# Optimization experiments

Measured on AMD Instinct MI355X. Metric: run time of the kernel, lower is better.

The kernel has to match this reference:

```python
import jax, jax.numpy as jnp
import numpy as np
import math

D = 1024
H = 16
B = 4
N = 2048


def setup_inputs() -> dict:
    key = jax.random.key(0)
    ks = jax.random.split(key, 10)
    scale_qkv = 0.01
    def kaiming_uniform(k, shape, scale):
        # attenuated_kaiming_uniform_: fan_in = shape[1], gain for leaky_relu a=sqrt(5)
        fan_in = shape[1]
        gain = math.sqrt(2.0 / (1 + 5.0))
        bound = math.sqrt(3.0) * gain * scale / math.sqrt(fan_in)
        return jax.random.uniform(k, shape, jnp.float32, -bound, bound)
    return {
        "x_q": jax.random.normal(ks[0], (B, N, D), jnp.float32),
        "x_kv": jax.random.normal(ks[1], (B, N, D), jnp.float32),
        "Wq": kaiming_uniform(ks[2], (D, D), scale_qkv),
        "bq": jnp.zeros((D,), jnp.float32),
        "Wk": kaiming_uniform(ks[3], (D, D), scale_qkv),
        "bk": jnp.zeros((D,), jnp.float32),
        "Wv": kaiming_uniform(ks[4], (D, D), scale_qkv),
        "bv": jnp.zeros((D,), jnp.float32),
        "Wo": kaiming_uniform(ks[5], (D, D), 1.0),
        "bo": jnp.zeros((D,), jnp.float32),
    }


def reference(x_q, x_kv, Wq, bq, Wk, bk, Wv, bv, Wo, bo):
    bs, n, d = x_q.shape
    hd = d // H  # head dim
    # torch Linear: y = x @ W^T + b
    q = x_q @ Wq.T + bq
    k = x_kv @ Wk.T + bk
    v = x_kv @ Wv.T + bv
    # reshape to [bs, H, n, hd]
    q = q.reshape(bs, n, H, hd).transpose(0, 2, 1, 3)
    k = k.reshape(bs, n, H, hd).transpose(0, 2, 1, 3)
    v = v.reshape(bs, n, H, hd).transpose(0, 2, 1, 3)
    scores = jnp.einsum("bhqd,bhkd->bhqk", q, k) / math.sqrt(hd)
    seq_ids = jnp.arange(n)
    causal = (seq_ids[None, :] <= seq_ids[:, None]).astype(scores.dtype)  # [n, n]
    scores = scores + (1.0 - causal) * -10000.0
    probs = jax.nn.softmax(scores, axis=-1)
    out = jnp.einsum("bhqk,bhkd->bhqd", probs, v)
    out = out.transpose(0, 2, 1, 3).reshape(bs, n, d)
    return out @ Wo.T + bo
```

## Files before the change

### kernel.cpp

```cpp
#include <hip/hip_runtime.h>

typedef unsigned short u16;
typedef unsigned int u32;
typedef __attribute__((ext_vector_type(8))) short short8;
typedef __attribute__((ext_vector_type(4))) float f32x4;

#define ASYNC_CP16(gsrc, ldst) \
  __builtin_amdgcn_global_load_lds((__attribute__((address_space(1))) void*)(gsrc), \
                                   (__attribute__((address_space(3))) void*)(ldst), 16, 0, 0)

static __device__ __forceinline__ u16 f2bf(float f) {
  u32 u = __builtin_bit_cast(u32, f);
  u = u + 0x7fffu + ((u >> 16) & 1u);
  return (u16)(u >> 16);
}
static __device__ __forceinline__ u32 pk2(float a, float b) {
  return (u32)f2bf(a) | ((u32)f2bf(b) << 16);
}
static __device__ __forceinline__ u32 pk2r(float a, float b) {
  u32 ua = __builtin_bit_cast(u32, a) + 0x8000u;
  u32 ub = __builtin_bit_cast(u32, b) + 0x8000u;
  return __builtin_amdgcn_perm(ub, ua, 0x07060302);
}

__global__ __launch_bounds__(256) void convert_all(
    const float* __restrict__ xq, const float* __restrict__ xkv,
    const float* __restrict__ wq, const float* __restrict__ wk,
    const float* __restrict__ wv, const float* __restrict__ wo,
    u16* __restrict__ dst)
{
  long i = ((long)blockIdx.x * 256 + threadIdx.x) * 4;
  const float* s; long o;
  if      (i < 8388608)  { s = xq;  o = i; }
  else if (i < 16777216) { s = xkv; o = i - 8388608; }
  else if (i < 17825792) { s = wq;  o = i - 16777216; }
  else if (i < 18874368) { s = wk;  o = i - 17825792; }
  else if (i < 19922944) { s = wv;  o = i - 18874368; }
  else                   { s = wo;  o = i - 19922944; }
  float4 v = *(const float4*)(s + o);
  uint2 pkv; pkv.x = pk2(v.x, v.y); pkv.y = pk2(v.z, v.w);
  *(uint2*)(dst + i) = pkv;
}

template<int EPI>
__global__ __launch_bounds__(256)
void gemm_k(const u16* __restrict__ Axq, const u16* __restrict__ Axkv,
            const u16* __restrict__ W0, const u16* __restrict__ W1, const u16* __restrict__ W2,
            const float* __restrict__ b0, const float* __restrict__ b1, const float* __restrict__ b2,
            u16* __restrict__ Qo, u16* __restrict__ Ko, u16* __restrict__ Vo,
            float* __restrict__ Fo)
{
  __shared__ u16 lsa[128*32];
  __shared__ u16 lsb[128*32];
  const int tid = threadIdx.x;
  const int w = tid >> 6, lane = tid & 63;
  const int wr = w >> 1, wc = w & 1;
  const int bm = blockIdx.x, bn = blockIdx.y, z = blockIdx.z;
  const int l15 = lane & 15, l4 = lane >> 4;

  const u16* A; const u16* W; const float* bias;
  if (EPI == 0) {
    A    = (z == 0) ? Axq : Axkv;
    W    = (z == 0) ? W0 : (z == 1) ? W1 : W2;
    bias = (z == 0) ? b0 : (z == 1) ? b1 : b2;
  } else {
    A = Axq; W = W0; bias = b0;
  }
  const u16* Ag = A + (long)bm*128*1024;
  const u16* Wg = W + (long)bn*128*1024;

  f32x4 acc[4][4];
#pragma unroll
  for (int i = 0; i < 4; ++i)
#pragma unroll
    for (int j = 0; j < 4; ++j)
      acc[i][j] = (f32x4){0.f,0.f,0.f,0.f};

  for (int k0 = 0; k0 < 1024; k0 += 32) {
    __syncthreads();
#pragma unroll
    for (int c = 0; c < 2; ++c) {
      int tp = c*256 + tid;
      int row = tp >> 2, col = (tp & 3) * 8;
      ASYNC_CP16(Ag + (long)row*1024 + k0 + col, &lsa[tp*8]);
      ASYNC_CP16(Wg + (long)row*1024 + k0 + col, &lsb[tp*8]);
    }
    __syncthreads();
    short8 af[4], bfr[4];
#pragma unroll
    for (int i = 0; i < 4; ++i)
      af[i] = *(const short8*)&lsa[(wr*64 + i*16 + l15)*32 + l4*8];
#pragma unroll
    for (int j = 0; j < 4; ++j)
      bfr[j] = *(const short8*)&lsb[(wc*64 + j*16 + l15)*32 + l4*8];
#pragma unroll
    for (int i = 0; i < 4; ++i)
#pragma unroll
      for (int j = 0; j < 4; ++j)
        acc[i][j] = __builtin_amdgcn_mfma_f32_16x16x32_bf16(af[i], bfr[j], acc[i][j], 0, 0, 0);
  }

#pragma unroll
  for (int j = 0; j < 4; ++j) {
    const int colg = bn*128 + wc*64 + j*16 + l15;
    const float bb = bias[colg];
#pragma unroll
    for (int i = 0; i < 4; ++i) {
      const int rowg = bm*128 + wr*64 + i*16 + l4*4;
      if (EPI == 1) {
#pragma unroll
        for (int r = 0; r < 4; ++r)
          Fo[(long)(rowg + r)*1024 + colg] = acc[i][j][r] + bb;
      } else {
        const int b  = rowg >> 11, n0 = rowg & 2047;
        const int h  = colg >> 6,  c  = colg & 63;
        const int bh = b*16 + h;
        const long hb = (long)bh*131072 + (long)(n0 >> 7)*8192;
        if (z == 0) {
#pragma unroll
          for (int r = 0; r < 4; ++r)
            Qo[((long)bh*2048 + n0 + r)*64 + c] = f2bf((acc[i][j][r] + bb) * 0.18033688f);
        } else if (z == 1) {
          const long base = hb + (long)(c >> 3)*1024 + (n0 & 127)*8 + (c & 7);
#pragma unroll
          for (int r = 0; r < 4; ++r)
            Ko[base + r*8] = f2bf(acc[i][j][r] + bb);
        } else {
          const long base = hb + (long)((n0 & 127) >> 3)*512 + (long)c*8 + (n0 & 7);
          uint2 pkv;
          pkv.x = pk2(acc[i][j][0] + bb, acc[i][j][1] + bb);
          pkv.y = pk2(acc[i][j][2] + bb, acc[i][j][3] + bb);
          *(uint2*)(Vo + base) = pkv;
        }
      }
    }
  }
}

__global__ __launch_bounds__(256)
void attn_k(const u16* __restrict__ Q, const u16* __restrict__ K,
            const u16* __restrict__ V, u16* __restrict__ AO)
{
  __shared__ u16 lk[8192];
  __shared__ u16 lv[8192];
  __shared__ u16 lp[4][1024];
  const int tid = threadIdx.x;
  const int w = tid >> 6, lane = tid & 63;
  const int l15 = lane & 15, l4 = lane >> 4;
  const int qt = (gridDim.x - 1) - blockIdx.x;
  const int bh = blockIdx.y;
  const int q0 = qt*64;
  const int qg = q0 + w*16 + l15;
  const u16* Qh = Q + (long)bh*131072;
  const u16* Kh = K + (long)bh*131072;
  const u16* Vh = V + (long)bh*131072;

  short8 qf[2];
#pragma unroll
  for (int ks = 0; ks < 2; ++ks)
    qf[ks] = *(const short8*)&Qh[(long)qg*64 + ks*32 + l4*8];

  f32x4 o[4];
#pragma unroll
  for (int nt = 0; nt < 4; ++nt) o[nt] = (f32x4){0.f,0.f,0.f,0.f};
  float rsum = 0.f;

  u16* pw = &lp[w][0];
  const int swz_q = (l15 & 7);
  const int ktmax = (q0 + 63) >> 7;
  for (int kt = 0; kt <= ktmax; ++kt) {
    __syncthreads();
#pragma unroll
    for (int c = 0; c < 4; ++c) {
      int tp = c*256 + tid;
      ASYNC_CP16(Kh + (long)kt*8192 + tp*8, &lk[tp*8]);
      ASYNC_CP16(Vh + (long)kt*8192 + tp*8, &lv[tp*8]);
    }
    __syncthreads();

    f32x4 s[8];
#pragma unroll
    for (int nt = 0; nt < 8; ++nt) s[nt] = (f32x4){0.f,0.f,0.f,0.f};
#pragma unroll
    for (int ks = 0; ks < 2; ++ks)
#pragma unroll
      for (int nt = 0; nt < 8; ++nt) {
        short8 kf = *(const short8*)&lk[(ks*4 + l4)*1024 + (nt*16 + l15)*8];
        s[nt] = __builtin_amdgcn_mfma_f32_16x16x32_bf16(kf, qf[ks], s[nt], 0, 0, 0);
      }

    if (kt*128 + 127 > q0) {
      const int kb = kt*128 + l4*4;
#pragma unroll
      for (int nt = 0; nt < 8; ++nt)
#pragma unroll
        for (int r = 0; r < 4; ++r)
          if (kb + nt*16 + r > qg) s[nt][r] = -1e30f;
    }

    u32 pk[8][2];
#pragma unroll
    for (int nt = 0; nt < 8; ++nt) {
      float p0 = __builtin_amdgcn_exp2f(s[nt][0]);
      float p1 = __builtin_amdgcn_exp2f(s[nt][1]);
      float p2 = __builtin_amdgcn_exp2f(s[nt][2]);
      float p3 = __builtin_amdgcn_exp2f(s[nt][3]);
      rsum += (p0 + p1) + (p2 + p3);
      pk[nt][0] = pk2r(p0, p1);
      pk[nt][1] = pk2r(p2, p3);
    }

#pragma unroll
    for (int h = 0; h < 2; ++h) {
#pragma unroll
      for (int ntl = 0; ntl < 4; ++ntl) {
        const int chunk = ntl*2 + (l4 >> 1);
        const int swz = chunk ^ swz_q;
        uint2 pr; pr.x = pk[4*h + ntl][0]; pr.y = pk[4*h + ntl][1];
        *(uint2*)&pw[l15*64 + swz*8 + (l4 & 1)*4] = pr;
      }
#pragma unroll
      for (int ksl = 0; ksl < 2; ++ksl) {
        const int swz = (ksl*4 + l4) ^ swz_q;
        short8 pf = *(const short8*)&pw[l15*64 + swz*8];
        const int ksg = h*2 + ksl;
#pragma unroll
        for (int nt = 0; nt < 4; ++nt) {
          short8 vf = *(const short8*)&lv[(ksg*4 + l4)*512 + (nt*16 + l15)*8];
          o[nt] = __builtin_amdgcn_mfma_f32_16x16x32_bf16(vf, pf, o[nt], 0, 0, 0);
        }
      }
    }
  }

  rsum += __shfl_xor(rsum, 16, 64);
  rsum += __shfl_xor(rsum, 32, 64);

  const int b = bh >> 4, h = bh & 15;
  const float inv = 1.0f / rsum;
  const long tok = (long)b*2048 + qg;
#pragma unroll
  for (int nt = 0; nt < 4; ++nt) {
    uint2 pkv;
    pkv.x = pk2(o[nt][0]*inv, o[nt][1]*inv);
    pkv.y = pk2(o[nt][2]*inv, o[nt][3]*inv);
    *(uint2*)&AO[tok*1024 + h*64 + nt*16 + l4*4] = pkv;
  }
}

extern "C" void kernel_launch(void* const* d_in, const int* in_sizes, int n_in,
                              void* d_out, int out_size, void* d_ws, size_t ws_size,
                              hipStream_t stream)
{
  const float* xq  = (const float*)d_in[0];
  const float* xkv = (const float*)d_in[1];
  const float* Wq  = (const float*)d_in[2];
  const float* bq  = (const float*)d_in[3];
  const float* Wk  = (const float*)d_in[4];
  const float* bk  = (const float*)d_in[5];
  const float* Wv  = (const float*)d_in[6];
  const float* bv  = (const float*)d_in[7];
  const float* Wo  = (const float*)d_in[8];
  const float* bo  = (const float*)d_in[9];

  u16* ws    = (u16*)d_ws;
  u16* xq_b  = ws;
  u16* xkv_b = xq_b  + (1l<<23);
  u16* wq_b  = xkv_b + (1l<<23);
  u16* wk_b  = wq_b  + (1l<<20);
  u16* wv_b  = wk_b  + (1l<<20);
  u16* wo_b  = wv_b  + (1l<<20);
  u16* Qb    = wo_b  + (1l<<20);
  u16* Kb    = Qb    + (1l<<23);
  u16* Vb    = Kb    + (1l<<23);
  u16* Ab    = Vb    + (1l<<23);

  convert_all<<<20480, 256, 0, stream>>>(xq, xkv, Wq, Wk, Wv, Wo, ws);
  gemm_k<0><<<dim3(64,8,3), 256, 0, stream>>>(xq_b, xkv_b, wq_b, wk_b, wv_b,
                                              bq, bk, bv, Qb, Kb, Vb, nullptr);
  attn_k<<<dim3(32,64), 256, 0, stream>>>(Qb, Kb, Vb, Ab);
  gemm_k<1><<<dim3(64,8,1), 256, 0, stream>>>(Ab, nullptr, wo_b, nullptr, nullptr,
                                              bo, nullptr, nullptr,
                                              nullptr, nullptr, nullptr,
                                              (float*)d_out);
}
```

Baseline: 344.3 us.

## Double-buffer K/V tiles in attention and widen blocks to 128 queries

The attention kernel now runs 512 threads (8 waves) per block covering 128 query rows, and the grid's query-tile count is halved. K/V tiles are double-buffered in LDS: the next tile's async loads are issued before computing on the current tile, with waitcnt plus barrier standing in for the two syncthreads. The goal is to hide global-load latency and to reuse each K/V tile across twice as many queries. In exchange LDS use per block doubles, which lowers occupancy, and the block count drops to 1024, so causal load imbalance could matter more.

Result: faster. 323.5 us (-6.0%).

```diff
diff --git a/kernel.cpp b/kernel.cpp
--- a/kernel.cpp
+++ b/kernel.cpp
@@ -137,19 +137,19 @@
   }
 }
 
-__global__ __launch_bounds__(256)
+__global__ __launch_bounds__(512, 4)
 void attn_k(const u16* __restrict__ Q, const u16* __restrict__ K,
             const u16* __restrict__ V, u16* __restrict__ AO)
 {
-  __shared__ u16 lk[8192];
-  __shared__ u16 lv[8192];
-  __shared__ u16 lp[4][1024];
+  __shared__ u16 lk[2][8192];
+  __shared__ u16 lv[2][8192];
+  __shared__ u16 lp[8][1024];
   const int tid = threadIdx.x;
   const int w = tid >> 6, lane = tid & 63;
   const int l15 = lane & 15, l4 = lane >> 4;
   const int qt = (gridDim.x - 1) - blockIdx.x;
   const int bh = blockIdx.y;
-  const int q0 = qt*64;
+  const int q0 = qt*128;
   const int qg = q0 + w*16 + l15;
   const u16* Qh = Q + (long)bh*131072;
   const u16* Kh = K + (long)bh*131072;
@@ -167,16 +167,33 @@
 
   u16* pw = &lp[w][0];
   const int swz_q = (l15 & 7);
-  const int ktmax = (q0 + 63) >> 7;
+  const int ktmax = qt;
+
+#pragma unroll
+  for (int c = 0; c < 2; ++c) {
+    int tp = c*512 + tid;
+    ASYNC_CP16(Kh + tp*8, &lk[0][tp*8]);
+    ASYNC_CP16(Vh + tp*8, &lv[0][tp*8]);
+  }
+
   for (int kt = 0; kt <= ktmax; ++kt) {
-    __syncthreads();
-#pragma unroll
-    for (int c = 0; c < 4; ++c) {
-      int tp = c*256 + tid;
-      ASYNC_CP16(Kh + (long)kt*8192 + tp*8, &lk[tp*8]);
-      ASYNC_CP16(Vh + (long)kt*8192 + tp*8, &lv[tp*8]);
-    }
-    __syncthreads();
+    const int cur = kt & 1;
+    if (kt < ktmax) {
+      const long off = (long)(kt + 1)*8192;
+#pragma unroll
+      for (int c = 0; c < 2; ++c) {
+        int tp = c*512 + tid;
+        ASYNC_CP16(Kh + off + tp*8, &lk[cur^1][tp*8]);
+        ASYNC_CP16(Vh + off + tp*8, &lv[cur^1][tp*8]);
+      }
+      asm volatile("s_waitcnt vmcnt(4)" ::: "memory");
+    } else {
+      asm volatile("s_waitcnt vmcnt(0)" ::: "memory");
+    }
+    __builtin_amdgcn_s_barrier();
+
+    const u16* lkc = &lk[cur][0];
+    const u16* lvc = &lv[cur][0];
 
     f32x4 s[8];
 #pragma unroll
@@ -185,11 +202,11 @@
     for (int ks = 0; ks < 2; ++ks)
 #pragma unroll
       for (int nt = 0; nt < 8; ++nt) {
-        short8 kf = *(const short8*)&lk[(ks*4 + l4)*1024 + (nt*16 + l15)*8];
+        short8 kf = *(const short8*)&lkc[(ks*4 + l4)*1024 + (nt*16 + l15)*8];
         s[nt] = __builtin_amdgcn_mfma_f32_16x16x32_bf16(kf, qf[ks], s[nt], 0, 0, 0);
       }
 
-    if (kt*128 + 127 > q0) {
+    if (kt == ktmax) {
       const int kb = kt*128 + l4*4;
 #pragma unroll
       for (int nt = 0; nt < 8; ++nt)
@@ -226,11 +243,14 @@
         const int ksg = h*2 + ksl;
 #pragma unroll
         for (int nt = 0; nt < 4; ++nt) {
-          short8 vf = *(const short8*)&lv[(ksg*4 + l4)*512 + (nt*16 + l15)*8];
+          short8 vf = *(const short8*)&lvc[(ksg*4 + l4)*512 + (nt*16 + l15)*8];
           o[nt] = __builtin_amdgcn_mfma_f32_16x16x32_bf16(vf, pf, o[nt], 0, 0, 0);
         }
       }
     }
+
+    asm volatile("" ::: "memory");
+    __builtin_amdgcn_s_barrier();
   }
 
   rsum += __shfl_xor(rsum, 16, 64);
@@ -278,7 +298,7 @@
   convert_all<<<20480, 256, 0, stream>>>(xq, xkv, Wq, Wk, Wv, Wo, ws);
   gemm_k<0><<<dim3(64,8,3), 256, 0, stream>>>(xq_b, xkv_b, wq_b, wk_b, wv_b,
                                               bq, bk, bv, Qb, Kb, Vb, nullptr);
-  attn_k<<<dim3(32,64), 256, 0, stream>>>(Qb, Kb, Vb, Ab);
+  attn_k<<<dim3(16,64), 512, 0, stream>>>(Qb, Kb, Vb, Ab);
   gemm_k<1><<<dim3(64,8,1), 256, 0, stream>>>(Ab, nullptr, wo_b, nullptr, nullptr,
                                               bo, nullptr, nullptr,
                                               nullptr, nullptr, nullptr,
```
